# Performance work log

Measured on AMD Instinct MI355X. Metric: run time of the kernel, lower is better.

Reference implementation:

```python
import jax, jax.numpy as jnp
import numpy as np
from jax import lax

VOCAB, EMB, HID = 50257, 256, 256
B, T = 64, 2048

def setup_inputs() -> dict:
    key = jax.random.key(0)
    ks = jax.random.split(key, 6)
    s = 1.0 / np.sqrt(HID)
    return {
        "sequence": jax.random.randint(ks[0], (B, T), 0, VOCAB),
        "embedding": jax.random.normal(ks[1], (VOCAB, EMB), jnp.float32),
        "w_ih": jax.random.uniform(ks[2], (3 * HID, EMB), jnp.float32, -s, s),
        "w_hh": jax.random.uniform(ks[3], (3 * HID, HID), jnp.float32, -s, s),
        "b_ih": jax.random.uniform(ks[4], (3 * HID,), jnp.float32, -s, s),
        "b_hh": jax.random.uniform(ks[5], (3 * HID,), jnp.float32, -s, s),
    }

def reference(sequence, embedding, w_ih, w_hh, b_ih, b_hh):
    # sequence: [B,T] int tokens. Original loops per-timestep; math == one GRU pass.
    H = w_hh.shape[1]
    x = embedding[sequence]                       # [B,T,E]
    x = jnp.transpose(x, (1, 0, 2))               # [T,B,E] (time-major)
    # input-side gate pre-activations for all steps at once: [T,B,3H]
    gi = jnp.einsum('tbe,ge->tbg', x, w_ih) + b_ih

    def step(h, gi_t):
        gh = h @ w_hh.T + b_hh                    # [B,3H]
        i_r, i_z, i_n = jnp.split(gi_t, 3, axis=-1)
        h_r, h_z, h_n = jnp.split(gh, 3, axis=-1)
        r = jax.nn.sigmoid(i_r + h_r)
        z = jax.nn.sigmoid(i_z + h_z)
        n = jnp.tanh(i_n + r * h_n)
        h_new = (1.0 - z) * n + z * h
        return h_new, None

    h0 = jnp.zeros((sequence.shape[0], H), dtype=embedding.dtype)
    hT, _ = lax.scan(step, h0, gi)
    return hT[None]                                # [1,B,H] like torch GRU hidden
```

## Files before the change

kernel.cpp:

```cpp
#include <hip/hip_runtime.h>
#include <hip/hip_fp16.h>

#define TSEQ   2048
#define NB     64
#define NE     256
#define NH     256
#define NG     768
#define TCH    64
#define NCHUNK (TSEQ / TCH)
#define POOL_BYTES 87552

__global__ void prep_whh(const float* __restrict__ whh, unsigned int* __restrict__ w16) {
  int idx = blockIdx.x * 256 + threadIdx.x;
  if (idx >= 98304) return;
  int c  = idx & 3;
  int i  = (idx >> 2) & 15;
  int g  = (idx >> 6) % 3;
  int js = idx / 192;
  int s  = js & 1;
  int j  = js >> 1;
  int k  = s * 128 + i * 8 + 2 * c;
  const float* src = whh + (size_t)(g * 256 + j) * 256 + k;
  union { struct { _Float16 a, b; } h; unsigned int u; } cvt;
  cvt.h.a = (_Float16)src[0];
  cvt.h.b = (_Float16)src[1];
  w16[idx] = cvt.u;
}

#define DOT12(H0,H1,H2,H3,R0,R1,R2,R3,Z0,Z1,Z2,Z3,N0,N1,N2,N3) \
  "v_dot2_f32_f16 v16, v" H0 ", v" R0 ", v16\n\t" \
  "v_dot2_f32_f16 v17, v" H0 ", v" Z0 ", v17\n\t" \
  "v_dot2_f32_f16 v18, v" H0 ", v" N0 ", v18\n\t" \
  "v_dot2_f32_f16 v16, v" H1 ", v" R1 ", v16\n\t" \
  "v_dot2_f32_f16 v17, v" H1 ", v" Z1 ", v17\n\t" \
  "v_dot2_f32_f16 v18, v" H1 ", v" N1 ", v18\n\t" \
  "v_dot2_f32_f16 v16, v" H2 ", v" R2 ", v16\n\t" \
  "v_dot2_f32_f16 v17, v" H2 ", v" Z2 ", v17\n\t" \
  "v_dot2_f32_f16 v18, v" H2 ", v" N2 ", v18\n\t" \
  "v_dot2_f32_f16 v16, v" H3 ", v" R3 ", v16\n\t" \
  "v_dot2_f32_f16 v17, v" H3 ", v" Z3 ", v17\n\t" \
  "v_dot2_f32_f16 v18, v" H3 ", v" N3 ", v18\n\t"

#define RSTEP(O0,O1,O2,O3,O4,O5,O6,O7,O8,O9,O10,O11,O12,O13,O14,O15) \
  "global_load_dword v12, v3, %[gip]\n\t" \
  "global_load_dword v13, v3, %[gip] offset:1024\n\t" \
  "global_load_dword v14, v3, %[gip] offset:2048\n\t" \
  "v_add_u32 v3, 0x30000, v3\n\t" \
  "v_mov_b32 v16, 0\n\t" \
  "v_mov_b32 v17, 0\n\t" \
  "v_mov_b32 v18, 0\n\t" \
  "ds_read_b128 v[4:7], v2 offset:" O0 "\n\t" \
  "ds_read_b128 v[8:11], v2 offset:" O1 "\n\t" \
  "s_waitcnt lgkmcnt(1)\n\t" \
  DOT12("4","5","6","7",  "64","65","66","67",    "128","129","130","131","192","193","194","195") \
  "ds_read_b128 v[4:7], v2 offset:" O2 "\n\t" \
  "s_waitcnt lgkmcnt(1)\n\t" \
  DOT12("8","9","10","11","68","69","70","71",    "132","133","134","135","196","197","198","199") \
  "ds_read_b128 v[8:11], v2 offset:" O3 "\n\t" \
  "s_waitcnt lgkmcnt(1)\n\t" \
  DOT12("4","5","6","7",  "72","73","74","75",    "136","137","138","139","200","201","202","203") \
  "ds_read_b128 v[4:7], v2 offset:" O4 "\n\t" \
  "s_waitcnt lgkmcnt(1)\n\t" \
  DOT12("8","9","10","11","76","77","78","79",    "140","141","142","143","204","205","206","207") \
  "ds_read_b128 v[8:11], v2 offset:" O5 "\n\t" \
  "s_waitcnt lgkmcnt(1)\n\t" \
  DOT12("4","5","6","7",  "80","81","82","83",    "144","145","146","147","208","209","210","211") \
  "ds_read_b128 v[4:7], v2 offset:" O6 "\n\t" \
  "s_waitcnt lgkmcnt(1)\n\t" \
  DOT12("8","9","10","11","84","85","86","87",    "148","149","150","151","212","213","214","215") \
  "ds_read_b128 v[8:11], v2 offset:" O7 "\n\t" \
  "s_waitcnt lgkmcnt(1)\n\t" \
  DOT12("4","5","6","7",  "88","89","90","91",    "152","153","154","155","216","217","218","219") \
  "ds_read_b128 v[4:7], v2 offset:" O8 "\n\t" \
  "s_waitcnt lgkmcnt(1)\n\t" \
  DOT12("8","9","10","11","92","93","94","95",    "156","157","158","159","220","221","222","223") \
  "ds_read_b128 v[8:11], v2 offset:" O9 "\n\t" \
  "s_waitcnt lgkmcnt(1)\n\t" \
  DOT12("4","5","6","7",  "96","97","98","99",    "160","161","162","163","224","225","226","227") \
  "ds_read_b128 v[4:7], v2 offset:" O10 "\n\t" \
  "s_waitcnt lgkmcnt(1)\n\t" \
  DOT12("8","9","10","11","100","101","102","103","164","165","166","167","228","229","230","231") \
  "ds_read_b128 v[8:11], v2 offset:" O11 "\n\t" \
  "s_waitcnt lgkmcnt(1)\n\t" \
  DOT12("4","5","6","7",  "104","105","106","107","168","169","170","171","232","233","234","235") \
  "ds_read_b128 v[4:7], v2 offset:" O12 "\n\t" \
  "s_waitcnt lgkmcnt(1)\n\t" \
  DOT12("8","9","10","11","108","109","110","111","172","173","174","175","236","237","238","239") \
  "ds_read_b128 v[8:11], v2 offset:" O13 "\n\t" \
  "s_waitcnt lgkmcnt(1)\n\t" \
  DOT12("4","5","6","7",  "112","113","114","115","176","177","178","179","240","241","242","243") \
  "ds_read_b128 v[4:7], v2 offset:" O14 "\n\t" \
  "s_waitcnt lgkmcnt(1)\n\t" \
  DOT12("8","9","10","11","116","117","118","119","180","181","182","183","244","245","246","247") \
  "ds_read_b128 v[8:11], v2 offset:" O15 "\n\t" \
  "s_waitcnt lgkmcnt(1)\n\t" \
  DOT12("4","5","6","7",  "120","121","122","123","184","185","186","187","248","249","250","251") \
  "s_waitcnt lgkmcnt(0)\n\t" \
  DOT12("8","9","10","11","124","125","126","127","188","189","190","191","252","253","254","255")

#define REC_TAIL(WOF) \
  "ds_bpermute_b32 v20, v19, v16\n\t" \
  "ds_bpermute_b32 v21, v19, v17\n\t" \
  "ds_bpermute_b32 v22, v19, v18\n\t" \
  "s_waitcnt lgkmcnt(0)\n\t" \
  "v_add_f32 v16, v16, v20\n\t" \
  "v_add_f32 v17, v17, v21\n\t" \
  "v_add_f32 v18, v18, v22\n\t" \
  "s_waitcnt vmcnt(0)\n\t" \
  "v_add_f32 v20, v12, v16\n\t" \
  "v_mul_f32 v20, 0xbfb8aa3b, v20\n\t" \
  "v_exp_f32 v20, v20\n\t" \
  "s_nop 0\n\t" \
  "v_add_f32 v20, 1.0, v20\n\t" \
  "v_rcp_f32 v20, v20\n\t" \
  "s_nop 0\n\t" \
  "v_add_f32 v21, v13, v17\n\t" \
  "v_mul_f32 v21, 0xbfb8aa3b, v21\n\t" \
  "v_exp_f32 v21, v21\n\t" \
  "s_nop 0\n\t" \
  "v_add_f32 v21, 1.0, v21\n\t" \
  "v_rcp_f32 v21, v21\n\t" \
  "s_nop 0\n\t" \
  "v_add_f32 v22, v18, v28\n\t" \
  "v_fma_f32 v22, v20, v22, v14\n\t" \
  "v_min_f32 v22, 0x41700000, v22\n\t" \
  "v_mul_f32 v22, 0x4038aa3b, v22\n\t" \
  "v_exp_f32 v22, v22\n\t" \
  "s_nop 0\n\t" \
  "v_add_f32 v23, -1.0, v22\n\t" \
  "v_add_f32 v22, 1.0, v22\n\t" \
  "v_rcp_f32 v22, v22\n\t" \
  "s_nop 0\n\t" \
  "v_mul_f32 v22, v23, v22\n\t" \
  "v_sub_f32 v23, v24, v22\n\t" \
  "v_fma_f32 v24, v21, v23, v22\n\t" \
  "v_cvt_f16_f32 v25, v24\n\t" \
  "ds_write_b16 v29, v25 offset:" WOF "\n\t" \
  "s_waitcnt lgkmcnt(0)\n\t" \
  "s_barrier\n\t"

#define WLD(D0,D1,OFF) \
  "global_load_dwordx4 v[" D0 ":" D1 "], %[wof], %[wptr] offset:" OFF "\n\t"

__global__ __launch_bounds__(512)
void fused_kernel(const int* __restrict__ seq, const float* __restrict__ emb,
                  const float* __restrict__ wih, const float* __restrict__ bih,
                  const float* __restrict__ bhh, const unsigned int* __restrict__ w16,
                  const float* __restrict__ rec_gi, float* __restrict__ gi_dst,
                  int gi_t0, float* __restrict__ h_state, float* __restrict__ out,
                  int rec_count, int chunk)
{
  __shared__ __align__(16) char smem[POOL_BYTES];
  const int tid = threadIdx.x;

  if ((int)blockIdx.x < rec_count) {
    const int b = blockIdx.x;
    const unsigned lane = tid & 63;
    const unsigned jj   = (unsigned)(tid >> 6) * 32 + (lane & 31);
    const unsigned sh   = lane >> 5;

    float h0 = 0.f;
    if (chunk != 0) h0 = h_state[b * NH + jj];
    const float bnv = bhh[2 * NH + jj];
    ((_Float16*)smem)[jj] = (_Float16)h0;
    __syncthreads();

    const unsigned pool0 = (unsigned)(uintptr_t)(smem);
    const unsigned hrd = pool0 + sh * 256;
    const unsigned hwa = pool0 + jj * 2;
    const unsigned gio = jj * 4;
    const unsigned bpa = (lane ^ 32u) << 2;
    const unsigned wof = (jj * 2 + sh) * 768;
    const float* gib = rec_gi + (size_t)b * NG;

    float hout;
    asm volatile(
      "v_mov_b32 v2, %[hrd]\n\t"
      "v_mov_b32 v3, %[gio]\n\t"
      "v_mov_b32 v19, %[bpa]\n\t"
      "v_mov_b32 v24, %[h0]\n\t"
      "v_mov_b32 v28, %[bn]\n\t"
      "v_mov_b32 v29, %[hwa]\n\t"
      WLD("64","67","0")    WLD("68","71","16")   WLD("72","75","32")   WLD("76","79","48")
      WLD("80","83","64")   WLD("84","87","80")   WLD("88","91","96")   WLD("92","95","112")
      WLD("96","99","128")  WLD("100","103","144")WLD("104","107","160")WLD("108","111","176")
      WLD("112","115","192")WLD("116","119","208")WLD("120","123","224")WLD("124","127","240")
      WLD("128","131","256")WLD("132","135","272")WLD("136","139","288")WLD("140","143","304")
      WLD("144","147","320")WLD("148","151","336")WLD("152","155","352")WLD("156","159","368")
      WLD("160","163","384")WLD("164","167","400")WLD("168","171","416")WLD("172","175","432")
      WLD("176","179","448")WLD("180","183","464")WLD("184","187","480")WLD("188","191","496")
      WLD("192","195","512")WLD("196","199","528")WLD("200","203","544")WLD("204","207","560")
      WLD("208","211","576")WLD("212","215","592")WLD("216","219","608")WLD("220","223","624")
      WLD("224","227","640")WLD("228","231","656")WLD("232","235","672")WLD("236","239","688")
      WLD("240","243","704")WLD("244","247","720")WLD("248","251","736")WLD("252","255","752")
      "s_waitcnt vmcnt(0)\n\t"
      "s_mov_b32 s20, 32\n\t"
      "1:\n\t"
      RSTEP("0","16","32","48","64","80","96","112",
            "128","144","160","176","192","208","224","240")
      REC_TAIL("512")
      RSTEP("512","528","544","560","576","592","608","624",
            "640","656","672","688","704","720","736","752")
      REC_TAIL("0")
      "s_sub_u32 s20, s20, 1\n\t"
      "s_cmp_lg_u32 s20, 0\n\t"
      "s_cbranch_scc1 1b\n\t"
      "v_mov_b32 %[hout], v24\n\t"
      : [hout] "=v"(hout)
      : [hrd] "v"(hrd), [gio] "v"(gio), [bpa] "v"(bpa), [h0] "v"(h0),
        [bn] "v"(bnv), [hwa] "v"(hwa), [wof] "v"(wof),
        [wptr] "s"(w16), [gip] "s"(gib)
      : "memory","scc","s20",
        "v2","v3","v4","v5","v6","v7","v8","v9","v10","v11","v12","v13","v14",
        "v16","v17","v18","v19","v20","v21","v22","v23","v24","v25","v28","v29",
        "v64","v65","v66","v67","v68","v69","v70","v71","v72","v73","v74","v75",
        "v76","v77","v78","v79","v80","v81","v82","v83","v84","v85","v86","v87",
        "v88","v89","v90","v91","v92","v93","v94","v95","v96","v97","v98","v99",
        "v100","v101","v102","v103","v104","v105","v106","v107","v108","v109",
        "v110","v111","v112","v113","v114","v115","v116","v117","v118","v119",
        "v120","v121","v122","v123","v124","v125","v126","v127","v128","v129",
        "v130","v131","v132","v133","v134","v135","v136","v137","v138","v139",
        "v140","v141","v142","v143","v144","v145","v146","v147","v148","v149",
        "v150","v151","v152","v153","v154","v155","v156","v157","v158","v159",
        "v160","v161","v162","v163","v164","v165","v166","v167","v168","v169",
        "v170","v171","v172","v173","v174","v175","v176","v177","v178","v179",
        "v180","v181","v182","v183","v184","v185","v186","v187","v188","v189",
        "v190","v191","v192","v193","v194","v195","v196","v197","v198","v199",
        "v200","v201","v202","v203","v204","v205","v206","v207","v208","v209",
        "v210","v211","v212","v213","v214","v215","v216","v217","v218","v219",
        "v220","v221","v222","v223","v224","v225","v226","v227","v228","v229",
        "v230","v231","v232","v233","v234","v235","v236","v237","v238","v239",
        "v240","v241","v242","v243","v244","v245","v246","v247","v248","v249",
        "v250","v251","v252","v253","v254","v255");

    h_state[b * NH + jj] = hout;
    if (out) out[b * NH + jj] = hout;
  } else {
    if (gi_dst == nullptr) return;
    float (*xs)[68]  = (float(*)[68])smem;
    float (*wsh)[68] = (float(*)[68])(smem + 17408);
    int*  tok        = (int*)(smem + 17408 + 69632);
    const int gb = blockIdx.x - rec_count;
    const int tl = gb & 63;
    const int g0 = (gb >> 6) * 256;
    const int t  = gi_t0 + tl;
    if (tid < 64) tok[tid] = seq[tid * TSEQ + t];
    const int tx = tid & 31;
    const int ty = tid >> 5;
    float acc[4][8];
#pragma unroll
    for (int i = 0; i < 4; ++i)
#pragma unroll
      for (int c8 = 0; c8 < 8; ++c8) acc[i][c8] = 0.f;

    for (int kb = 0; kb < 4; ++kb) {
      __syncthreads();
#pragma unroll
      for (int it = 0; it < 2; ++it) {
        int i = it * 512 + tid;
        int r = i >> 4, c = i & 15;
        *(float4*)(&xs[r][c * 4]) =
            *(const float4*)(emb + (size_t)tok[r] * NE + kb * 64 + c * 4);
      }
#pragma unroll
      for (int it = 0; it < 8; ++it) {
        int i = it * 512 + tid;
        int r = i >> 4, c = i & 15;
        *(float4*)(&wsh[r][c * 4]) =
            *(const float4*)(wih + (size_t)(g0 + r) * NE + kb * 64 + c * 4);
      }
      __syncthreads();
#pragma unroll 4
      for (int k4 = 0; k4 < 16; ++k4) {
        float4 xf[4], wf[8];
#pragma unroll
        for (int i = 0; i < 4; ++i) xf[i] = *(const float4*)(&xs[ty * 4 + i][k4 * 4]);
#pragma unroll
        for (int c8 = 0; c8 < 8; ++c8) wf[c8] = *(const float4*)(&wsh[tx + 32 * c8][k4 * 4]);
#pragma unroll
        for (int i = 0; i < 4; ++i)
#pragma unroll
          for (int c8 = 0; c8 < 8; ++c8)
            acc[i][c8] += xf[i].x * wf[c8].x + xf[i].y * wf[c8].y +
                          xf[i].z * wf[c8].z + xf[i].w * wf[c8].w;
      }
    }
#pragma unroll
    for (int i = 0; i < 4; ++i) {
      const int brow = ty * 4 + i;
      float* dst = gi_dst + ((size_t)(tl * NB + brow)) * NG + g0;
#pragma unroll
      for (int c8 = 0; c8 < 8; ++c8) {
        const int col = tx + 32 * c8;
        const int g = g0 + col;
        float bias = bih[g] + (g < 2 * NH ? bhh[g] : 0.f);
        dst[col] = acc[i][c8] + bias;
      }
    }
  }
}

extern "C" void kernel_launch(void* const* d_in, const int* in_sizes, int n_in,
                              void* d_out, int out_size, void* d_ws, size_t ws_size,
                              hipStream_t stream) {
  (void)in_sizes; (void)n_in; (void)out_size; (void)ws_size;
  const int*   seq = (const int*)d_in[0];
  const float* emb = (const float*)d_in[1];
  const float* wih = (const float*)d_in[2];
  const float* whh = (const float*)d_in[3];
  const float* bih = (const float*)d_in[4];
  const float* bhh = (const float*)d_in[5];
  float* out = (float*)d_out;
  char*  ws  = (char*)d_ws;

  unsigned int* w16     = (unsigned int*)(ws);
  float*        h_state = (float*)(ws + 393216);
  float*        gi0     = (float*)(ws + 458752);
  float*        gi1     = (float*)(ws + 458752 + 12582912);

  prep_whh<<<dim3(384), dim3(256), 0, stream>>>(whh, w16);

  fused_kernel<<<dim3(192), dim3(512), 0, stream>>>(
      seq, emb, wih, bih, bhh, w16,
      nullptr, gi0, 0, h_state, nullptr, 0, 0);

  for (int c = 0; c < NCHUNK; ++c) {
    float* rd  = (c & 1) ? gi1 : gi0;
    float* wr_ = (c & 1) ? gi0 : gi1;
    const bool last = (c == NCHUNK - 1);
    const int grid  = last ? NB : NB + 192;
    fused_kernel<<<dim3(grid), dim3(512), 0, stream>>>(
        seq, emb, wih, bih, bhh, w16,
        rd, last ? nullptr : wr_, (c + 1) * TCH, h_state,
        last ? out : nullptr, NB, c);
  }
}
```

Before: 2.599 ms.

## Use MFMA fp16 for input projection and scalar-broadcast h in recurrence

The input-gate projection blocks now convert embeddings and a pre-converted fp16 W_ih to fp16 in shared memory and compute with 16x16x32 MFMA instructions instead of fp32 FMA loops. The recurrent step is restructured so each wave reads its h slice once, broadcasts it via v_readlane into SGPRs and uses scalar-operand dot2. The cross-half reduction now goes through an LDS exchange with a barrier instead of ds_bpermute, and a few s_nops are rescheduled. This lowers input-projection precision to fp16 and adds an extra barrier per step, and the readlane sequence adds latency on the serial critical path.

```diff
diff --git a/kernel.cpp b/kernel.cpp
--- a/kernel.cpp
+++ b/kernel.cpp
@@ -8,40 +8,77 @@
 #define NG     768
 #define TCH    64
 #define NCHUNK (TSEQ / TCH)
-#define POOL_BYTES 87552
-
-__global__ void prep_whh(const float* __restrict__ whh, unsigned int* __restrict__ w16) {
+#define POOL_BYTES 103936
+
+typedef _Float16 f16x8 __attribute__((ext_vector_type(8)));
+typedef float    f32x4 __attribute__((ext_vector_type(4)));
+typedef unsigned u32x4 __attribute__((ext_vector_type(4)));
+
+__global__ void prep_whh(const float* __restrict__ whh, unsigned* __restrict__ w16) {
   int idx = blockIdx.x * 256 + threadIdx.x;
   if (idx >= 98304) return;
-  int c  = idx & 3;
-  int i  = (idx >> 2) & 15;
-  int g  = (idx >> 6) % 3;
-  int js = idx / 192;
-  int s  = js & 1;
-  int j  = js >> 1;
-  int k  = s * 128 + i * 8 + 2 * c;
+  int c    = idx & 3;
+  int i    = (idx >> 2) & 15;
+  int g    = (idx >> 6) % 3;
+  int rest = idx / 192;
+  int j    = rest & 255;
+  int s    = rest >> 8;
+  int k    = s * 128 + i * 8 + 2 * c;
   const float* src = whh + (size_t)(g * 256 + j) * 256 + k;
-  union { struct { _Float16 a, b; } h; unsigned int u; } cvt;
-  cvt.h.a = (_Float16)src[0];
-  cvt.h.b = (_Float16)src[1];
-  w16[idx] = cvt.u;
+  union { _Float16 h[2]; unsigned u; } p;
+  p.h[0] = (_Float16)src[0];
+  p.h[1] = (_Float16)src[1];
+  w16[idx] = p.u;
 }
 
-#define DOT12(H0,H1,H2,H3,R0,R1,R2,R3,Z0,Z1,Z2,Z3,N0,N1,N2,N3) \
-  "v_dot2_f32_f16 v16, v" H0 ", v" R0 ", v16\n\t" \
-  "v_dot2_f32_f16 v17, v" H0 ", v" Z0 ", v17\n\t" \
-  "v_dot2_f32_f16 v18, v" H0 ", v" N0 ", v18\n\t" \
-  "v_dot2_f32_f16 v16, v" H1 ", v" R1 ", v16\n\t" \
-  "v_dot2_f32_f16 v17, v" H1 ", v" Z1 ", v17\n\t" \
-  "v_dot2_f32_f16 v18, v" H1 ", v" N1 ", v18\n\t" \
-  "v_dot2_f32_f16 v16, v" H2 ", v" R2 ", v16\n\t" \
-  "v_dot2_f32_f16 v17, v" H2 ", v" Z2 ", v17\n\t" \
-  "v_dot2_f32_f16 v18, v" H2 ", v" N2 ", v18\n\t" \
-  "v_dot2_f32_f16 v16, v" H3 ", v" R3 ", v16\n\t" \
-  "v_dot2_f32_f16 v17, v" H3 ", v" Z3 ", v17\n\t" \
-  "v_dot2_f32_f16 v18, v" H3 ", v" N3 ", v18\n\t"
-
-#define RSTEP(O0,O1,O2,O3,O4,O5,O6,O7,O8,O9,O10,O11,O12,O13,O14,O15) \
+__global__ void prep_wih(const float* __restrict__ wih, unsigned* __restrict__ wih16) {
+  int idx = blockIdx.x * 256 + threadIdx.x;
+  if (idx >= 98304) return;
+  union { _Float16 h[2]; unsigned u; } p;
+  p.h[0] = (_Float16)wih[2 * idx];
+  p.h[1] = (_Float16)wih[2 * idx + 1];
+  wih16[idx] = p.u;
+}
+
+#define WLD(D0,D1,OFF) \
+  "global_load_dwordx4 v[" D0 ":" D1 "], %[wof], %[wptr] offset:" OFF "\n\t"
+
+#define RL4(Q,S0,S1,S2,S3) \
+  "v_readlane_b32 s" #S0 ", v32, " #Q "\n\t" \
+  "v_readlane_b32 s" #S1 ", v33, " #Q "\n\t" \
+  "v_readlane_b32 s" #S2 ", v34, " #Q "\n\t" \
+  "v_readlane_b32 s" #S3 ", v35, " #Q "\n\t"
+
+#define DQS(S,R,Z,N) \
+  "v_dot2_f32_f16 v16, s" #S ", v" #R ", v16\n\t" \
+  "v_dot2_f32_f16 v17, s" #S ", v" #Z ", v17\n\t" \
+  "v_dot2_f32_f16 v18, s" #S ", v" #N ", v18\n\t"
+
+#define RL_ALL \
+  RL4(0,36,37,38,39)   RL4(1,40,41,42,43)   RL4(2,44,45,46,47)   RL4(3,48,49,50,51) \
+  RL4(4,52,53,54,55)   RL4(5,56,57,58,59)   RL4(6,60,61,62,63)   RL4(7,64,65,66,67) \
+  RL4(8,68,69,70,71)   RL4(9,72,73,74,75)   RL4(10,76,77,78,79)  RL4(11,80,81,82,83) \
+  RL4(12,84,85,86,87)  RL4(13,88,89,90,91)  RL4(14,92,93,94,95)  RL4(15,96,97,98,99)
+
+#define DQ_ALL \
+  DQS(36,64,128,192) DQS(37,65,129,193) DQS(38,66,130,194) DQS(39,67,131,195) \
+  DQS(40,68,132,196) DQS(41,69,133,197) DQS(42,70,134,198) DQS(43,71,135,199) \
+  DQS(44,72,136,200) DQS(45,73,137,201) DQS(46,74,138,202) DQS(47,75,139,203) \
+  DQS(48,76,140,204) DQS(49,77,141,205) DQS(50,78,142,206) DQS(51,79,143,207) \
+  DQS(52,80,144,208) DQS(53,81,145,209) DQS(54,82,146,210) DQS(55,83,147,211) \
+  DQS(56,84,148,212) DQS(57,85,149,213) DQS(58,86,150,214) DQS(59,87,151,215) \
+  DQS(60,88,152,216) DQS(61,89,153,217) DQS(62,90,154,218) DQS(63,91,155,219) \
+  DQS(64,92,156,220) DQS(65,93,157,221) DQS(66,94,158,222) DQS(67,95,159,223) \
+  DQS(68,96,160,224) DQS(69,97,161,225) DQS(70,98,162,226) DQS(71,99,163,227) \
+  DQS(72,100,164,228) DQS(73,101,165,229) DQS(74,102,166,230) DQS(75,103,167,231) \
+  DQS(76,104,168,232) DQS(77,105,169,233) DQS(78,106,170,234) DQS(79,107,171,235) \
+  DQS(80,108,172,236) DQS(81,109,173,237) DQS(82,110,174,238) DQS(83,111,175,239) \
+  DQS(84,112,176,240) DQS(85,113,177,241) DQS(86,114,178,242) DQS(87,115,179,243) \
+  DQS(88,116,180,244) DQS(89,117,181,245) DQS(90,118,182,246) DQS(91,119,183,247) \
+  DQS(92,120,184,248) DQS(93,121,185,249) DQS(94,122,186,250) DQS(95,123,187,251) \
+  DQS(96,124,188,252) DQS(97,125,189,253) DQS(98,126,190,254) DQS(99,127,191,255)
+
+#define STEP(BUF,NBUF) \
   "global_load_dword v12, v3, %[gip]\n\t" \
   "global_load_dword v13, v3, %[gip] offset:1024\n\t" \
   "global_load_dword v14, v3, %[gip] offset:2048\n\t" \
@@ -49,59 +86,18 @@
   "v_mov_b32 v16, 0\n\t" \
   "v_mov_b32 v17, 0\n\t" \
   "v_mov_b32 v18, 0\n\t" \
-  "ds_read_b128 v[4:7], v2 offset:" O0 "\n\t" \
-  "ds_read_b128 v[8:11], v2 offset:" O1 "\n\t" \
-  "s_waitcnt lgkmcnt(1)\n\t" \
-  DOT12("4","5","6","7",  "64","65","66","67",    "128","129","130","131","192","193","194","195") \
-  "ds_read_b128 v[4:7], v2 offset:" O2 "\n\t" \
-  "s_waitcnt lgkmcnt(1)\n\t" \
-  DOT12("8","9","10","11","68","69","70","71",    "132","133","134","135","196","197","198","199") \
-  "ds_read_b128 v[8:11], v2 offset:" O3 "\n\t" \
-  "s_waitcnt lgkmcnt(1)\n\t" \
-  DOT12("4","5","6","7",  "72","73","74","75",    "136","137","138","139","200","201","202","203") \
-  "ds_read_b128 v[4:7], v2 offset:" O4 "\n\t" \
-  "s_waitcnt lgkmcnt(1)\n\t" \
-  DOT12("8","9","10","11","76","77","78","79",    "140","141","142","143","204","205","206","207") \
-  "ds_read_b128 v[8:11], v2 offset:" O5 "\n\t" \
-  "s_waitcnt lgkmcnt(1)\n\t" \
-  DOT12("4","5","6","7",  "80","81","82","83",    "144","145","146","147","208","209","210","211") \
-  "ds_read_b128 v[4:7], v2 offset:" O6 "\n\t" \
-  "s_waitcnt lgkmcnt(1)\n\t" \
-  DOT12("8","9","10","11","84","85","86","87",    "148","149","150","151","212","213","214","215") \
-  "ds_read_b128 v[8:11], v2 offset:" O7 "\n\t" \
-  "s_waitcnt lgkmcnt(1)\n\t" \
-  DOT12("4","5","6","7",  "88","89","90","91",    "152","153","154","155","216","217","218","219") \
-  "ds_read_b128 v[4:7], v2 offset:" O8 "\n\t" \
-  "s_waitcnt lgkmcnt(1)\n\t" \
-  DOT12("8","9","10","11","92","93","94","95",    "156","157","158","159","220","221","222","223") \
-  "ds_read_b128 v[8:11], v2 offset:" O9 "\n\t" \
-  "s_waitcnt lgkmcnt(1)\n\t" \
-  DOT12("4","5","6","7",  "96","97","98","99",    "160","161","162","163","224","225","226","227") \
-  "ds_read_b128 v[4:7], v2 offset:" O10 "\n\t" \
-  "s_waitcnt lgkmcnt(1)\n\t" \
-  DOT12("8","9","10","11","100","101","102","103","164","165","166","167","228","229","230","231") \
-  "ds_read_b128 v[8:11], v2 offset:" O11 "\n\t" \
-  "s_waitcnt lgkmcnt(1)\n\t" \
-  DOT12("4","5","6","7",  "104","105","106","107","168","169","170","171","232","233","234","235") \
-  "ds_read_b128 v[4:7], v2 offset:" O12 "\n\t" \
-  "s_waitcnt lgkmcnt(1)\n\t" \
-  DOT12("8","9","10","11","108","109","110","111","172","173","174","175","236","237","238","239") \
-  "ds_read_b128 v[8:11], v2 offset:" O13 "\n\t" \
-  "s_waitcnt lgkmcnt(1)\n\t" \
-  DOT12("4","5","6","7",  "112","113","114","115","176","177","178","179","240","241","242","243") \
-  "ds_read_b128 v[4:7], v2 offset:" O14 "\n\t" \
-  "s_waitcnt lgkmcnt(1)\n\t" \
-  DOT12("8","9","10","11","116","117","118","119","180","181","182","183","244","245","246","247") \
-  "ds_read_b128 v[8:11], v2 offset:" O15 "\n\t" \
-  "s_waitcnt lgkmcnt(1)\n\t" \
-  DOT12("4","5","6","7",  "120","121","122","123","184","185","186","187","248","249","250","251") \
+  "ds_read_b128 v[32:35], v2 offset:" BUF "\n\t" \
   "s_waitcnt lgkmcnt(0)\n\t" \
-  DOT12("8","9","10","11","124","125","126","127","188","189","190","191","252","253","254","255")
-
-#define REC_TAIL(WOF) \
-  "ds_bpermute_b32 v20, v19, v16\n\t" \
-  "ds_bpermute_b32 v21, v19, v17\n\t" \
-  "ds_bpermute_b32 v22, v19, v18\n\t" \
+  RL_ALL \
+  DQ_ALL \
+  "ds_write_b32 v29, v16\n\t" \
+  "ds_write_b32 v29, v17 offset:1024\n\t" \
+  "ds_write_b32 v29, v18 offset:2048\n\t" \
+  "s_waitcnt lgkmcnt(0)\n\t" \
+  "s_barrier\n\t" \
+  "ds_read_b32 v20, v30\n\t" \
+  "ds_read_b32 v21, v30 offset:1024\n\t" \
+  "ds_read_b32 v22, v30 offset:2048\n\t" \
   "s_waitcnt lgkmcnt(0)\n\t" \
   "v_add_f32 v16, v16, v20\n\t" \
   "v_add_f32 v17, v17, v21\n\t" \
@@ -110,42 +106,35 @@
   "v_add_f32 v20, v12, v16\n\t" \
   "v_mul_f32 v20, 0xbfb8aa3b, v20\n\t" \
   "v_exp_f32 v20, v20\n\t" \
-  "s_nop 0\n\t" \
-  "v_add_f32 v20, 1.0, v20\n\t" \
-  "v_rcp_f32 v20, v20\n\t" \
-  "s_nop 0\n\t" \
   "v_add_f32 v21, v13, v17\n\t" \
   "v_mul_f32 v21, 0xbfb8aa3b, v21\n\t" \
   "v_exp_f32 v21, v21\n\t" \
-  "s_nop 0\n\t" \
+  "v_add_f32 v20, 1.0, v20\n\t" \
+  "v_rcp_f32 v20, v20\n\t" \
   "v_add_f32 v21, 1.0, v21\n\t" \
   "v_rcp_f32 v21, v21\n\t" \
-  "s_nop 0\n\t" \
   "v_add_f32 v22, v18, v28\n\t" \
   "v_fma_f32 v22, v20, v22, v14\n\t" \
   "v_min_f32 v22, 0x41700000, v22\n\t" \
   "v_mul_f32 v22, 0x4038aa3b, v22\n\t" \
   "v_exp_f32 v22, v22\n\t" \
-  "s_nop 0\n\t" \
+  "s_nop 1\n\t" \
   "v_add_f32 v23, -1.0, v22\n\t" \
   "v_add_f32 v22, 1.0, v22\n\t" \
   "v_rcp_f32 v22, v22\n\t" \
-  "s_nop 0\n\t" \
+  "s_nop 1\n\t" \
   "v_mul_f32 v22, v23, v22\n\t" \
   "v_sub_f32 v23, v24, v22\n\t" \
   "v_fma_f32 v24, v21, v23, v22\n\t" \
   "v_cvt_f16_f32 v25, v24\n\t" \
-  "ds_write_b16 v29, v25 offset:" WOF "\n\t" \
+  "ds_write_b16 v31, v25 offset:" NBUF "\n\t" \
   "s_waitcnt lgkmcnt(0)\n\t" \
   "s_barrier\n\t"
 
-#define WLD(D0,D1,OFF) \
-  "global_load_dwordx4 v[" D0 ":" D1 "], %[wof], %[wptr] offset:" OFF "\n\t"
-
 __global__ __launch_bounds__(512)
 void fused_kernel(const int* __restrict__ seq, const float* __restrict__ emb,
-                  const float* __restrict__ wih, const float* __restrict__ bih,
-                  const float* __restrict__ bhh, const unsigned int* __restrict__ w16,
+                  const unsigned* __restrict__ wih16, const float* __restrict__ bih,
+                  const float* __restrict__ bhh, const unsigned* __restrict__ w16,
                   const float* __restrict__ rec_gi, float* __restrict__ gi_dst,
                   int gi_t0, float* __restrict__ h_state, float* __restrict__ out,
                   int rec_count, int chunk)
@@ -154,33 +143,36 @@
   const int tid = threadIdx.x;
 
   if ((int)blockIdx.x < rec_count) {
-    const int b = blockIdx.x;
-    const unsigned lane = tid & 63;
-    const unsigned jj   = (unsigned)(tid >> 6) * 32 + (lane & 31);
-    const unsigned sh   = lane >> 5;
+    const int b    = blockIdx.x;
+    const int lane = tid & 63;
+    const int w    = tid >> 6;
+    const int s_   = w >> 2;
+    const int j    = (w & 3) * 64 + lane;
 
     float h0 = 0.f;
-    if (chunk != 0) h0 = h_state[b * NH + jj];
-    const float bnv = bhh[2 * NH + jj];
-    ((_Float16*)smem)[jj] = (_Float16)h0;
+    if (chunk != 0) h0 = h_state[b * NH + j];
+    const float bnv = bhh[2 * NH + j];
+    ((_Float16*)smem)[j] = (_Float16)h0;
     __syncthreads();
 
     const unsigned pool0 = (unsigned)(uintptr_t)(smem);
-    const unsigned hrd = pool0 + sh * 256;
-    const unsigned hwa = pool0 + jj * 2;
-    const unsigned gio = jj * 4;
-    const unsigned bpa = (lane ^ 32u) << 2;
-    const unsigned wof = (jj * 2 + sh) * 768;
+    const unsigned hrd = pool0 + s_ * 256 + (lane & 15) * 16;
+    const unsigned hwa = pool0 + j * 2;
+    const unsigned pwr = pool0 + 2048 + s_ * 3072 + j * 4;
+    const unsigned prd = pool0 + 2048 + (1 - s_) * 3072 + j * 4;
+    const unsigned gio = j * 4;
+    const unsigned wof = (unsigned)(s_ * 256 + j) * 768;
     const float* gib = rec_gi + (size_t)b * NG;
 
     float hout;
     asm volatile(
       "v_mov_b32 v2, %[hrd]\n\t"
       "v_mov_b32 v3, %[gio]\n\t"
-      "v_mov_b32 v19, %[bpa]\n\t"
       "v_mov_b32 v24, %[h0]\n\t"
       "v_mov_b32 v28, %[bn]\n\t"
-      "v_mov_b32 v29, %[hwa]\n\t"
+      "v_mov_b32 v29, %[pwr]\n\t"
+      "v_mov_b32 v30, %[prd]\n\t"
+      "v_mov_b32 v31, %[hwa]\n\t"
       WLD("64","67","0")    WLD("68","71","16")   WLD("72","75","32")   WLD("76","79","48")
       WLD("80","83","64")   WLD("84","87","80")   WLD("88","91","96")   WLD("92","95","112")
       WLD("96","99","128")  WLD("100","103","144")WLD("104","107","160")WLD("108","111","176")
@@ -196,23 +188,25 @@
       "s_waitcnt vmcnt(0)\n\t"
       "s_mov_b32 s20, 32\n\t"
       "1:\n\t"
-      RSTEP("0","16","32","48","64","80","96","112",
-            "128","144","160","176","192","208","224","240")
-      REC_TAIL("512")
-      RSTEP("512","528","544","560","576","592","608","624",
-            "640","656","672","688","704","720","736","752")
-      REC_TAIL("0")
+      STEP("0","1024")
+      STEP("1024","0")
       "s_sub_u32 s20, s20, 1\n\t"
       "s_cmp_lg_u32 s20, 0\n\t"
       "s_cbranch_scc1 1b\n\t"
       "v_mov_b32 %[hout], v24\n\t"
       : [hout] "=v"(hout)
-      : [hrd] "v"(hrd), [gio] "v"(gio), [bpa] "v"(bpa), [h0] "v"(h0),
-        [bn] "v"(bnv), [hwa] "v"(hwa), [wof] "v"(wof),
+      : [hrd] "v"(hrd), [gio] "v"(gio), [h0] "v"(h0), [bn] "v"(bnv),
+        [pwr] "v"(pwr), [prd] "v"(prd), [hwa] "v"(hwa), [wof] "v"(wof),
         [wptr] "s"(w16), [gip] "s"(gib)
       : "memory","scc","s20",
-        "v2","v3","v4","v5","v6","v7","v8","v9","v10","v11","v12","v13","v14",
-        "v16","v17","v18","v19","v20","v21","v22","v23","v24","v25","v28","v29",
+        "s36","s37","s38","s39","s40","s41","s42","s43","s44","s45","s46","s47",
+        "s48","s49","s50","s51","s52","s53","s54","s55","s56","s57","s58","s59",
+        "s60","s61","s62","s63","s64","s65","s66","s67","s68","s69","s70","s71",
+        "s72","s73","s74","s75","s76","s77","s78","s79","s80","s81","s82","s83",
+        "s84","s85","s86","s87","s88","s89","s90","s91","s92","s93","s94","s95",
+        "s96","s97","s98","s99",
+        "v2","v3","v12","v13","v14","v16","v17","v18","v20","v21","v22","v23",
+        "v24","v25","v28","v29","v30","v31","v32","v33","v34","v35",
         "v64","v65","v66","v67","v68","v69","v70","v71","v72","v73","v74","v75",
         "v76","v77","v78","v79","v80","v81","v82","v83","v84","v85","v86","v87",
         "v88","v89","v90","v91","v92","v93","v94","v95","v96","v97","v98","v99",
@@ -233,69 +227,80 @@
         "v240","v241","v242","v243","v244","v245","v246","v247","v248","v249",
         "v250","v251","v252","v253","v254","v255");
 
-    h_state[b * NH + jj] = hout;
-    if (out) out[b * NH + jj] = hout;
+    h_state[b * NH + j] = hout;
+    if (out) out[b * NH + j] = hout;
   } else {
     if (gi_dst == nullptr) return;
-    float (*xs)[68]  = (float(*)[68])smem;
-    float (*wsh)[68] = (float(*)[68])(smem + 17408);
-    int*  tok        = (int*)(smem + 17408 + 69632);
+    _Float16* xs   = (_Float16*)smem;
+    _Float16* wsh  = (_Float16*)(smem + 33792);
+    int*      tok  = (int*)(smem + 103424);
     const int gb = blockIdx.x - rec_count;
     const int tl = gb & 63;
     const int g0 = (gb >> 6) * 256;
     const int t  = gi_t0 + tl;
     if (tid < 64) tok[tid] = seq[tid * TSEQ + t];
-    const int tx = tid & 31;
-    const int ty = tid >> 5;
-    float acc[4][8];
-#pragma unroll
-    for (int i = 0; i < 4; ++i)
-#pragma unroll
-      for (int c8 = 0; c8 < 8; ++c8) acc[i][c8] = 0.f;
-
-    for (int kb = 0; kb < 4; ++kb) {
-      __syncthreads();
-#pragma unroll
-      for (int it = 0; it < 2; ++it) {
-        int i = it * 512 + tid;
-        int r = i >> 4, c = i & 15;
-        *(float4*)(&xs[r][c * 4]) =
-            *(const float4*)(emb + (size_t)tok[r] * NE + kb * 64 + c * 4);
+    __syncthreads();
+
+    {
+      const int r = tid >> 3, cb = tid & 7;
+      const float* src = emb + (size_t)tok[r] * NE + cb * 32;
+      _Float16* dst = xs + r * 264 + cb * 32;
+#pragma unroll
+      for (int m = 0; m < 8; ++m) {
+        float4 v = *(const float4*)(src + m * 4);
+        union { _Float16 h[4]; uint2 u; } p;
+        p.h[0] = (_Float16)v.x; p.h[1] = (_Float16)v.y;
+        p.h[2] = (_Float16)v.z; p.h[3] = (_Float16)v.w;
+        *(uint2*)(dst + m * 4) = p.u;
       }
-#pragma unroll
-      for (int it = 0; it < 8; ++it) {
-        int i = it * 512 + tid;
-        int r = i >> 4, c = i & 15;
-        *(float4*)(&wsh[r][c * 4]) =
-            *(const float4*)(wih + (size_t)(g0 + r) * NE + kb * 64 + c * 4);
+    }
+
+    const int w  = tid >> 6, l = tid & 63;
+    const int lr = l & 15, lk = (l >> 4) * 8;
+    f32x4 acc[4][2] = {};
+
+#pragma unroll
+    for (int kh = 0; kh < 2; ++kh) {
+      {
+        if (kh) __syncthreads();
+        const int g = tid >> 1, hb = tid & 1;
+        const unsigned* srcu = wih16 + ((size_t)(g0 + g) * 128 + kh * 64 + hb * 32);
+        _Float16* dsth = wsh + g * 136 + hb * 64;
+#pragma unroll
+        for (int i = 0; i < 8; ++i)
+          *(u32x4*)(dsth + i * 8) = *(const u32x4*)(srcu + i * 4);
       }
       __syncthreads();
-#pragma unroll 4
-      for (int k4 = 0; k4 < 16; ++k4) {
-        float4 xf[4], wf[8];
-#pragma unroll
-        for (int i = 0; i < 4; ++i) xf[i] = *(const float4*)(&xs[ty * 4 + i][k4 * 4]);
-#pragma unroll
-        for (int c8 = 0; c8 < 8; ++c8) wf[c8] = *(const float4*)(&wsh[tx + 32 * c8][k4 * 4]);
-#pragma unroll
-        for (int i = 0; i < 4; ++i)
-#pragma unroll
-          for (int c8 = 0; c8 < 8; ++c8)
-            acc[i][c8] += xf[i].x * wf[c8].x + xf[i].y * wf[c8].y +
-                          xf[i].z * wf[c8].z + xf[i].w * wf[c8].w;
+#pragma unroll
+      for (int ks = 0; ks < 4; ++ks) {
+        f16x8 a[4], bfr[2];
+#pragma unroll
+        for (int mt = 0; mt < 4; ++mt)
+          a[mt] = *(const f16x8*)(xs + (mt * 16 + lr) * 264 + kh * 128 + ks * 32 + lk);
+#pragma unroll
+        for (int n = 0; n < 2; ++n)
+          bfr[n] = *(const f16x8*)(wsh + ((w * 2 + n) * 16 + lr) * 136 + ks * 32 + lk);
+#pragma unroll
+        for (int mt = 0; mt < 4; ++mt)
+#pragma unroll
+          for (int n = 0; n < 2; ++n)
+            acc[mt][n] = __builtin_amdgcn_mfma_f32_16x16x32_f16(
+                a[mt], bfr[n], acc[mt][n], 0, 0, 0);
       }
     }
-#pragma unroll
-    for (int i = 0; i < 4; ++i) {
-      const int brow = ty * 4 + i;
-      float* dst = gi_dst + ((size_t)(tl * NB + brow)) * NG + g0;
-#pragma unroll
-      for (int c8 = 0; c8 < 8; ++c8) {
-        const int col = tx + 32 * c8;
-        const int g = g0 + col;
-        float bias = bih[g] + (g < 2 * NH ? bhh[g] : 0.f);
-        dst[col] = acc[i][c8] + bias;
-      }
+
+    const int rbase = (l >> 4) * 4;
+#pragma unroll
+    for (int n = 0; n < 2; ++n) {
+      const int gcol = g0 + (w * 2 + n) * 16 + lr;
+      const float bias = bih[gcol] + (gcol < 2 * NH ? bhh[gcol] : 0.f);
+#pragma unroll
+      for (int mt = 0; mt < 4; ++mt)
+#pragma unroll
+        for (int rr = 0; rr < 4; ++rr) {
+          const int brow = mt * 16 + rbase + rr;
+          gi_dst[((size_t)tl * NB + brow) * NG + gcol] = acc[mt][n][rr] + bias;
+        }
     }
   }
 }
@@ -313,15 +318,17 @@
   float* out = (float*)d_out;
   char*  ws  = (char*)d_ws;
 
-  unsigned int* w16     = (unsigned int*)(ws);
-  float*        h_state = (float*)(ws + 393216);
-  float*        gi0     = (float*)(ws + 458752);
-  float*        gi1     = (float*)(ws + 458752 + 12582912);
+  unsigned* w16     = (unsigned*)(ws);
+  unsigned* wih16   = (unsigned*)(ws + 393216);
+  float*    h_state = (float*)(ws + 786432);
+  float*    gi0     = (float*)(ws + 851968);
+  float*    gi1     = (float*)(ws + 851968 + 12582912);
 
   prep_whh<<<dim3(384), dim3(256), 0, stream>>>(whh, w16);
+  prep_wih<<<dim3(384), dim3(256), 0, stream>>>(wih, wih16);
 
   fused_kernel<<<dim3(192), dim3(512), 0, stream>>>(
-      seq, emb, wih, bih, bhh, w16,
+      seq, emb, wih16, bih, bhh, w16,
       nullptr, gi0, 0, h_state, nullptr, 0, 0);
 
   for (int c = 0; c < NCHUNK; ++c) {
@@ -330,7 +337,7 @@
     const bool last = (c == NCHUNK - 1);
     const int grid  = last ? NB : NB + 192;
     fused_kernel<<<dim3(grid), dim3(512), 0, stream>>>(
-        seq, emb, wih, bih, bhh, w16,
+        seq, emb, wih16, bih, bhh, w16,
         rd, last ? nullptr : wr_, (c + 1) * TCH, h_state,
         last ? out : nullptr, NB, c);
   }
```

After: 2.975 ms. +14.5%, slower.
